# Kernel optimization log

Measured on AMD Instinct MI355X. Metric: run time of the kernel, lower is better.

The kernel has to match this reference:

```python
import jax, jax.numpy as jnp
from jax import lax
import numpy as np

B, N, C = 4, 2000, 80           # images, proposals/img, foreground classes
SCORE_THR = 0.05
IOU_THR = 0.5
MAX_PER_IMG = 100
K_PRE = 2000                     # pre-NMS top-k candidates per image
STDS = np.array([0.1, 0.1, 0.2, 0.2], dtype=np.float32)
MAX_RATIO = float(abs(np.log(16.0 / 1000.0)))  # wh_ratio_clip=16/1000


def setup_inputs() -> dict:
    key = jax.random.key(0)
    k1, k2, k3 = jax.random.split(key, 3)
    class_outs = jax.random.normal(k1, (B, N, C + 1), dtype=jnp.float32)
    regression_outs = jax.random.normal(k2, (B, N, C * 4), dtype=jnp.float32) * 0.5
    # random valid proposal boxes inside 800x1333 images (x1<x2, y1<y2)
    xy = jax.random.uniform(k3, (B, N, 2, 2), dtype=jnp.float32)
    xy = xy * jnp.array([1333.0, 800.0], dtype=jnp.float32)
    lo = jnp.min(xy, axis=2)
    hi = jnp.max(xy, axis=2) + 1.0
    boxes = jnp.concatenate([lo, hi], axis=-1)  # [B,N,4] x1,y1,x2,y2
    images_hw = jnp.tile(jnp.array([[800, 1333]], dtype=jnp.int32), (B, 1))
    return {"class_outs": class_outs, "regression_outs": regression_outs,
            "boxes": boxes, "images_hw": images_hw}


def _decode(props, deltas, h, w):
    # props [N,4], deltas [N,C,4] -> decoded boxes [N,C,4], clipped to image
    d = deltas * jnp.asarray(STDS)
    dx, dy, dw, dh = d[..., 0], d[..., 1], d[..., 2], d[..., 3]
    dw = jnp.clip(dw, -MAX_RATIO, MAX_RATIO)
    dh = jnp.clip(dh, -MAX_RATIO, MAX_RATIO)
    px = (props[:, None, 0] + props[:, None, 2]) * 0.5
    py = (props[:, None, 1] + props[:, None, 3]) * 0.5
    pw = props[:, None, 2] - props[:, None, 0]
    ph = props[:, None, 3] - props[:, None, 1]
    gx = px + pw * dx
    gy = py + ph * dy
    gw = pw * jnp.exp(dw)
    gh = ph * jnp.exp(dh)
    x1 = jnp.clip(gx - gw * 0.5, 0.0, w)
    y1 = jnp.clip(gy - gh * 0.5, 0.0, h)
    x2 = jnp.clip(gx + gw * 0.5, 0.0, w)
    y2 = jnp.clip(gy + gh * 0.5, 0.0, h)
    return jnp.stack([x1, y1, x2, y2], axis=-1)


def _pairwise_iou(b):
    # b [K,4] -> iou [K,K]
    area = (b[:, 2] - b[:, 0]) * (b[:, 3] - b[:, 1])
    lt = jnp.maximum(b[:, None, :2], b[None, :, :2])
    rb = jnp.minimum(b[:, None, 2:], b[None, :, 2:])
    wh = jnp.clip(rb - lt, 0.0)
    inter = wh[..., 0] * wh[..., 1]
    return inter / (area[:, None] + area[None, :] - inter + 1e-6)


def _process_image(cls_out, reg_out, props, hw):
    h = hw[0].astype(jnp.float32)
    w = hw[1].astype(jnp.float32)
    scores = jax.nn.softmax(cls_out, axis=-1)[:, :C]          # drop background col
    bboxes = _decode(props, reg_out.reshape(N, C, 4), h, w)   # [N,C,4]
    flat_scores = scores.reshape(-1)                          # [N*C]
    flat_boxes = bboxes.reshape(-1, 4)
    labels = jnp.tile(jnp.arange(C, dtype=jnp.int32), N)      # class fastest-varying
    cand = jnp.where(flat_scores > SCORE_THR, flat_scores, -1.0)
    top_scores, top_idx = lax.top_k(cand, K_PRE)
    top_boxes = flat_boxes[top_idx]
    top_labels = labels[top_idx]
    valid = top_scores > SCORE_THR
    # class-offset trick: boxes of distinct classes never overlap
    off = top_labels.astype(jnp.float32)[:, None] * (jnp.maximum(h, w) + 1.0)
    iou = _pairwise_iou(top_boxes + off)                      # [K_PRE,K_PRE]
    idxs = jnp.arange(K_PRE)

    def body(i, keep):
        sup = (idxs > i) & (iou[i] > IOU_THR) & keep[i]
        return keep & ~sup

    keep = lax.fori_loop(0, K_PRE, body, valid)
    kept_scores = jnp.where(keep, top_scores, -1.0)
    det_scores, det_i = lax.top_k(kept_scores, MAX_PER_IMG)
    det_valid = det_scores > SCORE_THR
    det_boxes = jnp.where(det_valid[:, None], top_boxes[det_i], 0.0)
    det_labels = jnp.where(det_valid, top_labels[det_i], -1)
    det_scores = jnp.where(det_valid, det_scores, 0.0)
    return det_boxes, det_scores, det_labels


def reference(class_outs, regression_outs, boxes, images_hw):
    det_boxes, det_scores, det_labels = jax.vmap(_process_image)(
        class_outs, regression_outs, boxes, images_hw)
    return det_boxes, det_scores, det_labels
```

## Files before the change

kernel.cpp:

```cpp
#include <hip/hip_runtime.h>


typedef unsigned long long u64;
typedef unsigned int u32;

#define B_ 4
#define N_ 2000
#define C_ 80
#define NCLS 81
#define KPRE 2000
#define MAXDET 100
#define TARGET 192
#define NB 2312
#define NBPAD 2368
#define NG 37
#define HBASE 0xF500
#define KSHIFT 46
#define CAPA 256
#define CAPB 2048
#define CAPBLK 128
#define BPI 125
#define SPW 9
#define BIGI 0x7fffffff

#define WS_GCNT  0
#define WS_GKEYS 2048
#define WS_GFLAG 514048
#define WS_GHIST 514064

__device__ __forceinline__ u64 pack_key(float score, unsigned fi) {
  return ((u64)__float_as_uint(score) << 32) | (u64)(0xFFFFFFFFu - fi);
}
__device__ __forceinline__ int bucket_of_bits(u32 sb) {
  return min(max((int)(sb >> 14) - HBASE, 0), NB - 1);
}

__device__ __forceinline__ float wred_max(float v) {
  int t;
#define STEPM(ctrl)                                                          \
  t = __builtin_amdgcn_update_dpp(__float_as_int(v), __float_as_int(v),      \
                                  (ctrl), 0xF, 0xF, false);                  \
  v = fmaxf(v, __int_as_float(t));
  STEPM(0x111) STEPM(0x112) STEPM(0x114) STEPM(0x118) STEPM(0x142) STEPM(0x143)
#undef STEPM
  return __int_as_float(__builtin_amdgcn_readlane(__float_as_int(v), 63));
}
__device__ __forceinline__ float wred_sum(float v) {
  int t;
#define STEPS(ctrl)                                                          \
  t = __builtin_amdgcn_update_dpp(0, __float_as_int(v), (ctrl), 0xF, 0xF,    \
                                  false);                                    \
  v = v + __int_as_float(t);
  STEPS(0x111) STEPS(0x112) STEPS(0x114) STEPS(0x118) STEPS(0x142) STEPS(0x143)
#undef STEPS
  return __int_as_float(__builtin_amdgcn_readlane(__float_as_int(v), 63));
}

__device__ __forceinline__ int dpp_min8(int v) {
  int t;
  t = __builtin_amdgcn_update_dpp(BIGI, v, 0x104, 0xF, 0xF, false);
  v = min(v, t);
  t = __builtin_amdgcn_update_dpp(BIGI, v, 0x102, 0xF, 0xF, false);
  v = min(v, t);
  t = __builtin_amdgcn_update_dpp(BIGI, v, 0x101, 0xF, 0xF, false);
  v = min(v, t);
  return v;
}

__device__ __forceinline__ float4 decode_one(
    u64 kk, const float* __restrict__ reg, const float* __restrict__ props,
    int b, float h, float w, float offscale) {
  const float MAXR = 4.135166556742356f;
  unsigned fi = 0xFFFFFFFFu - (u32)kk;
  int n = (int)(fi / (unsigned)C_);
  int c = (int)(fi - (unsigned)n * (unsigned)C_);
  float4 p = ((const float4*)props)[b * N_ + n];
  const float* dl = reg + ((size_t)(b * N_ + n)) * (C_ * 4) + c * 4;
  float dx = dl[0] * 0.1f;
  float dy = dl[1] * 0.1f;
  float dw = fminf(fmaxf(dl[2] * 0.2f, -MAXR), MAXR);
  float dh = fminf(fmaxf(dl[3] * 0.2f, -MAXR), MAXR);
  float px = (p.x + p.z) * 0.5f, py = (p.y + p.w) * 0.5f;
  float pw = p.z - p.x, ph = p.w - p.y;
  float gx = px + pw * dx, gy = py + ph * dy;
  float gw = pw * expf(dw), gh = ph * expf(dh);
  float off = (float)c * offscale;
  return make_float4(fminf(fmaxf(gx - gw * 0.5f, 0.0f), w) + off,
                     fminf(fmaxf(gy - gh * 0.5f, 0.0f), h) + off,
                     fminf(fmaxf(gx + gw * 0.5f, 0.0f), w) + off,
                     fminf(fmaxf(gy + gh * 0.5f, 0.0f), h) + off);
}

__global__ __launch_bounds__(1024) void cand_kernel(
    const float* __restrict__ cls, u64* __restrict__ gkeys,
    int* __restrict__ gcnt, u32* __restrict__ ghist) {
  __shared__ int s_wc[16], s_woff[16];
  const int tid = threadIdx.x;
  const int w = tid >> 6, lane = tid & 63;
  const int blk = blockIdx.x;
  const int b = blk / BPI;
  const int n = (blk % BPI) * 16 + w;
  const float* lg = cls + (size_t)(b * N_ + n) * NCLS;
  float x0 = lg[lane];
  float x1 = (lane < 17) ? lg[64 + lane] : -3.0e38f;
  float mx = wred_max(fmaxf(x0, x1));
  float e0 = expf(x0 - mx);
  float e1 = (lane < 17) ? expf(x1 - mx) : 0.0f;
  float sum = wred_sum(e0 + e1);
  float sc0 = e0 / sum, sc1 = e1 / sum;
  bool p0 = sc0 > 0.05f;
  bool p1 = (lane < 16) && (sc1 > 0.05f);
  u64 m0 = __ballot(p0), m1 = __ballot(p1);
  int c0 = __popcll(m0);
  if (lane == 0) s_wc[w] = c0 + __popcll(m1);
  __syncthreads();
  if (tid == 0) {
    int acc = 0;
#pragma unroll
    for (int i = 0; i < 16; ++i) { s_woff[i] = acc; acc += s_wc[i]; }
    gcnt[blk] = acc;
  }
  __syncthreads();
  const int base = s_woff[w];
  const u64 lt = (1ull << lane) - 1;
  u64* gk = gkeys + (size_t)blk * CAPBLK;
  u32* gh = ghist + (size_t)b * NBPAD;
  if (p0) {
    int slot = base + __popcll(m0 & lt);
    if (slot < CAPBLK) gk[slot] = pack_key(sc0, (unsigned)(n * C_ + lane));
    atomicAdd(&gh[bucket_of_bits(__float_as_uint(sc0))], 1u);
  }
  if (p1) {
    int slot = base + c0 + __popcll(m1 & lt);
    if (slot < CAPBLK) gk[slot] = pack_key(sc1, (unsigned)(n * C_ + 64 + lane));
    atomicAdd(&gh[bucket_of_bits(__float_as_uint(sc1))], 1u);
  }
}

__global__ __launch_bounds__(1024) void nmsA_kernel(
    const float* __restrict__ reg, const float* __restrict__ props,
    const int* __restrict__ hw, const u64* __restrict__ gkeys,
    const int* __restrict__ gcnt, const u32* __restrict__ ghist,
    int* __restrict__ gflag, float* __restrict__ out) {
  __shared__ u64 lds8[2156];
  char* bp = (char*)lds8;
  u64* SS = (u64*)bp;
  u64* U = (u64*)(bp + 2048);
  u64* rb = (u64*)(bp + 4128);
  float4* bxA = (float4*)(bp + 12320);
  int* outl = (int*)(bp + 16416);
  int* misc = (int*)(bp + 16928);
  int* s_coarse = (int*)(bp + 16992);

  const int b = blockIdx.x, tid = threadIdx.x;
  const int wv = tid >> 6, lane = tid & 63;

  float h = (float)hw[b * 2 + 0];
  float w = (float)hw[b * 2 + 1];
  float offscale = fmaxf(h, w) + 1.0f;

  if (tid < 16) misc[tid] = 0;
  if (tid >= NG && tid < 64) s_coarse[tid] = 0;

  int cnts[SPW];
  u64 ka[SPW], kb[SPW];
  if (wv < 14) {
#pragma unroll
    for (int k = 0; k < SPW; k++) {
      int p = wv * SPW + k;
      cnts[k] = (p < BPI) ? gcnt[b * BPI + p] : 0;
    }
#pragma unroll
    for (int k = 0; k < SPW; k++) {
      int p = wv * SPW + k;
      int cnt = min(cnts[k], CAPBLK);
      const u64* seg = gkeys + (size_t)(b * BPI + p) * CAPBLK;
      ka[k] = (lane < cnt) ? seg[lane] : 0ULL;
      kb[k] = (64 + lane < cnt) ? seg[64 + lane] : 0ULL;
    }
  } else {
    int g0 = (wv == 14) ? 0 : 19;
    int g1 = (wv == 14) ? 19 : NG;
    for (int g2 = g0; g2 < g1; g2++) {
      int v = (int)ghist[b * NBPAD + ((g2 << 6) | lane)];
#pragma unroll
      for (int o = 32; o; o >>= 1) v += __shfl_xor(v, o);
      if (lane == 0) s_coarse[g2] = v;
    }
  }
  __syncthreads();

  if (tid < 64) {
    int v = s_coarse[lane];
#pragma unroll
    for (int off = 1; off < 64; off <<= 1) {
      int src = lane + off;
      int o = __shfl(v, src < 64 ? src : 63);
      if (src < 64) v += o;
    }
    int Mtot = __shfl(v, 0);
    u64 pm = __ballot(v >= TARGET);
    int T_A = 0, S_A;
    if (pm) {
      int gs = 63 - __builtin_clzll(pm);
      int beyond = __shfl(v, gs + 1);
      int fv = (int)ghist[b * NBPAD + ((gs << 6) | lane)];
#pragma unroll
      for (int off = 1; off < 64; off <<= 1) {
        int src = lane + off;
        int o = __shfl(fv, src < 64 ? src : 63);
        if (src < 64) fv += o;
      }
      int cum = beyond + fv;
      u64 pm2 = __ballot(cum >= TARGET);
      int tr = 63 - __builtin_clzll(pm2);
      T_A = (gs << 6) + tr;
      S_A = __shfl(cum, tr);
    } else {
      S_A = Mtot;
    }
    if (lane == 0) { misc[0] = T_A; misc[2] = S_A; misc[3] = Mtot; }
  }
  __syncthreads();

  const int T_A = misc[0], S_A = misc[2], Mtot = misc[3];
  bool modeB = (S_A > CAPA);
  int K = 0, nkept = 0;

  if (!modeB) {
    if (wv < 14) {
      bool ovf = false;
      const u64 lt = (1ull << lane) - 1;
#pragma unroll
      for (int k = 0; k < SPW; k++) {
        int cnt = cnts[k];
        if (cnt > CAPBLK) { ovf = true; cnt = CAPBLK; }
        bool pr = (lane < cnt) &&
                  (bucket_of_bits((u32)(ka[k] >> 32)) >= T_A);
        u64 mk = __ballot(pr);
        if (mk) {
          int wbase = 0;
          if (lane == 0) wbase = atomicAdd(&misc[4], __popcll(mk));
          wbase = __shfl(wbase, 0);
          if (pr) {
            int pos = wbase + __popcll(mk & lt);
            if (pos < CAPA) U[pos] = ka[k];
          }
        }
        pr = (64 + lane < cnt) &&
             (bucket_of_bits((u32)(kb[k] >> 32)) >= T_A);
        mk = __ballot(pr);
        if (mk) {
          int wbase = 0;
          if (lane == 0) wbase = atomicAdd(&misc[4], __popcll(mk));
          wbase = __shfl(wbase, 0);
          if (pr) {
            int pos = wbase + __popcll(mk & lt);
            if (pos < CAPA) U[pos] = kb[k];
          }
        }
      }
      if (lane == 0 && ovf) misc[7] = 1;
    }
    __syncthreads();
    if (misc[7]) modeB = true;
    int S = misc[4];
    if (S > CAPA) S = CAPA;

    if (!modeB) {
      if (tid == 0 && (S & 1)) U[S] = 0ULL;
      __syncthreads();
      if (tid < S) {
        u64 k1 = U[tid];
        int r1 = 0;
        const ulonglong2* Uu2 = (const ulonglong2*)U;
        int half = (S + 1) >> 1;
        for (int k = 0; k < half; k++) {
          ulonglong2 kk = Uu2[k];
          r1 += (kk.x > k1) + (kk.y > k1);
        }
        SS[r1] = k1;
      }
      __syncthreads();
      K = S;
      for (int j = tid; j < K; j += 1024)
        bxA[j] = decode_one(SS[j], reg, props, b, h, w, offscale);
      __syncthreads();

      int nwords = (S + 63) >> 6;
      int ntiles = nwords * (nwords + 1) / 2;
      for (int t = wv; t < ntiles; t += 16) {
        int ti = 0, rem = t;
        while (rem >= nwords - ti) { rem -= nwords - ti; ti++; }
        int tj = ti + rem;
        int i = (ti << 6) + lane;
        float4 bi4 = bxA[i];
        float ai = (bi4.z - bi4.x) * (bi4.w - bi4.y);
        u64 bits = 0;
        int jbase = tj << 6;
        int jcount = min(64, S - jbase);
        for (int jj = 0; jj < jcount; jj++) {
          int j = jbase + jj;
          float4 bj = bxA[j];
          float aj = (bj.z - bj.x) * (bj.w - bj.y);
          float iw = fmaxf(fminf(bi4.z, bj.z) - fmaxf(bi4.x, bj.x), 0.0f);
          float ih = fmaxf(fminf(bi4.w, bj.w) - fmaxf(bi4.y, bj.y), 0.0f);
          float inter = iw * ih;
          float iou = inter / (ai + aj - inter + 1e-6f);
          if (j > i && iou > 0.5f) bits |= (1ull << jj);
        }
        if (i < S) rb[i * 4 + tj] = bits;
      }
      __syncthreads();

      if (tid < 64) {
        int nw7 = (S + 63) >> 6;
        u64 alive = 0;
        if (lane < nw7) {
          alive = ~0ull;
          int remb = S & 63;
          if (lane == nw7 - 1 && remb) alive = (1ull << remb) - 1;
        }
        int nk = 0;
        if (S > 0) {
          int i = 0;
          u64 row = (lane < nw7) ? rb[0 * 4 + lane] : 0ull;
          for (;;) {
            if (lane == 0) outl[nk] = i;
            nk++;
            if (nk >= MAXDET) break;
            if (lane == (i >> 6)) alive &= ~(1ull << (i & 63));
            u64 rowSpec = (i + 1 < S && lane < nw7) ? rb[(i + 1) * 4 + lane] : 0ull;
            u64 a2 = alive & ~row;
            alive = a2;
            int cnd = a2 ? ((lane << 6) + (int)__builtin_ctzll(a2)) : BIGI;
            int m8 = dpp_min8(cnd);
            int ni = __builtin_amdgcn_readfirstlane(m8);
            if (ni >= BIGI) break;
            row = (ni == i + 1) ? rowSpec
                                : ((lane < nw7) ? rb[ni * 4 + lane] : 0ull);
            i = ni;
          }
        }
        if (lane == 0) misc[6] = nk;
      }
      __syncthreads();
      nkept = misc[6];
      if (nkept < MAXDET && K < Mtot && K < KPRE) modeB = true;
    }
  }

  if (tid == 0) gflag[b] = modeB ? 1 : 0;
  if (modeB) return;

  float* oBox = out;
  float* oSc = out + B_ * MAXDET * 4;
  float* oLb = out + B_ * MAXDET * 5;
  for (int k2 = tid; k2 < MAXDET; k2 += 1024) {
    float4 bb = make_float4(0.0f, 0.0f, 0.0f, 0.0f);
    float sv = 0.0f, lv = -1.0f;
    if (k2 < nkept) {
      int idx = outl[k2];
      u64 kk = SS[idx];
      sv = __uint_as_float((u32)(kk >> 32));
      unsigned fi = 0xFFFFFFFFu - (u32)kk;
      int c = (int)(fi % (unsigned)C_);
      float off = (float)c * offscale;
      float4 ob = bxA[idx];
      bb = make_float4(ob.x - off, ob.y - off, ob.z - off, ob.w - off);
      lv = (float)c;
    }
    oBox[(b * MAXDET + k2) * 4 + 0] = bb.x;
    oBox[(b * MAXDET + k2) * 4 + 1] = bb.y;
    oBox[(b * MAXDET + k2) * 4 + 2] = bb.z;
    oBox[(b * MAXDET + k2) * 4 + 3] = bb.w;
    oSc[b * MAXDET + k2] = sv;
    oLb[b * MAXDET + k2] = lv;
  }
}

__global__ __launch_bounds__(1024) void nmsB_kernel(
    const float* __restrict__ reg, const float* __restrict__ props,
    const int* __restrict__ hw, const u64* __restrict__ gkeys,
    const int* __restrict__ gcnt, const int* __restrict__ gflag,
    float* __restrict__ out) {
  const int b = blockIdx.x, tid = threadIdx.x;
  if (gflag[b] == 0) return;

  __shared__ u64 lds8[7952];
  char* bp = (char*)lds8;
  u32* hist = (u32*)(bp + 0);
  u64* U2 = (u64*)(bp + 9472);
  u64* SSB = (u64*)(bp + 25856);
  int* outl = (int*)(bp + 42240);
  int* misc = (int*)(bp + 42752);
  const int wv = tid >> 6, lane = tid & 63;

  float h = (float)hw[b * 2 + 0];
  float w = (float)hw[b * 2 + 1];
  float offscale = fmaxf(h, w) + 1.0f;

  for (int i = tid; i < NBPAD; i += 1024) hist[i] = 0;
  if (tid < 16) misc[tid] = 0;
  __syncthreads();

  for (int k = 0; k < 8; k++) {
    int p = wv + 16 * k;
    if (p >= BPI) break;
    int cnt = min(gcnt[b * BPI + p], CAPBLK);
    const u64* seg = gkeys + (size_t)(b * BPI + p) * CAPBLK;
#pragma unroll
    for (int r = 0; r < 2; r++) {
      int idx = lane + 64 * r;
      if (idx < cnt) {
        u64 key = seg[idx];
        int bi = min(max((int)(key >> KSHIFT) - HBASE, 0), NB - 1);
        atomicAdd(&hist[bi], 1u);
      }
    }
  }
  __syncthreads();

  if (tid == 0) {
    int acc = 0, tb = 0;
    for (int bi = NB - 1; bi >= 0; bi--) {
      acc += (int)hist[bi];
      if (acc >= KPRE) { tb = bi; break; }
    }
    if (acc > CAPB) tb = min(tb + 1, NB - 1);
    misc[1] = tb;
    misc[4] = 0;
  }
  __syncthreads();
  int T_B = misc[1];

  for (int k = 0; k < 8; k++) {
    int p = wv + 16 * k;
    if (p >= BPI) break;
    int cnt = min(gcnt[b * BPI + p], CAPBLK);
    const u64* seg = gkeys + (size_t)(b * BPI + p) * CAPBLK;
#pragma unroll
    for (int r = 0; r < 2; r++) {
      int idx = lane + 64 * r;
      bool pred = false;
      u64 key = 0;
      if (idx < cnt) {
        key = seg[idx];
        int bi = min(max((int)(key >> KSHIFT) - HBASE, 0), NB - 1);
        pred = (bi >= T_B);
      }
      u64 mk = __ballot(pred);
      if (mk) {
        int wbase = 0;
        if (lane == 0) wbase = atomicAdd(&misc[4], __popcll(mk));
        wbase = __shfl(wbase, 0);
        if (pred) {
          int pos = wbase + __popcll(mk & ((1ull << lane) - 1));
          if (pos < CAPB) U2[pos] = key;
        }
      }
    }
  }
  __syncthreads();
  int S = misc[4];
  if (S > CAPB) S = CAPB;
  {
    int j1 = tid, j2 = tid + 1024;
    u64 k1 = (j1 < S) ? U2[j1] : 0ULL;
    u64 k2 = (j2 < S) ? U2[j2] : 0ULL;
    int r1 = 0, r2 = 0;
    for (int k = 0; k < S; k++) {
      u64 kk = U2[k];
      r1 += (kk > k1);
      r2 += (kk > k2);
    }
    __syncthreads();
    if (j1 < S) SSB[r1] = k1;
    if (j2 < S) SSB[r2] = k2;
  }
  __syncthreads();
  int K = (S < KPRE) ? S : KPRE;
  int j1 = tid, j2 = tid + 1024;
  bool kp1 = (j1 < K), kp2 = (j2 < K);
  float4 bb1 = kp1 ? decode_one(SSB[j1], reg, props, b, h, w, offscale)
                   : make_float4(0, 0, 0, 0);
  float4 bb2 = kp2 ? decode_one(SSB[j2], reg, props, b, h, w, offscale)
                   : make_float4(0, 0, 0, 0);
  int nk = 0;
  if (K > 0) {
    int i = 0;
    for (;;) {
      if (tid == 0) { outl[nk] = i; misc[5] = K; }
      nk++;
      if (nk >= MAXDET) break;
      __syncthreads();
      float4 tb = decode_one(SSB[i], reg, props, b, h, w, offscale);
      float ai = (tb.z - tb.x) * (tb.w - tb.y);
      int ln = K;
      if (kp1 && j1 > i) {
        float aj = (bb1.z - bb1.x) * (bb1.w - bb1.y);
        float iw = fmaxf(fminf(tb.z, bb1.z) - fmaxf(tb.x, bb1.x), 0.0f);
        float ih = fmaxf(fminf(tb.w, bb1.w) - fmaxf(tb.y, bb1.y), 0.0f);
        float inter = iw * ih;
        float iou = inter / (ai + aj - inter + 1e-6f);
        if (iou > 0.5f) kp1 = false;
        else ln = min(ln, j1);
      }
      if (kp2 && j2 > i) {
        float aj = (bb2.z - bb2.x) * (bb2.w - bb2.y);
        float iw = fmaxf(fminf(tb.z, bb2.z) - fmaxf(tb.x, bb2.x), 0.0f);
        float ih = fmaxf(fminf(tb.w, bb2.w) - fmaxf(tb.y, bb2.y), 0.0f);
        float inter = iw * ih;
        float iou = inter / (ai + aj - inter + 1e-6f);
        if (iou > 0.5f) kp2 = false;
        else ln = min(ln, j2);
      }
#pragma unroll
      for (int off = 32; off; off >>= 1) ln = min(ln, __shfl_xor(ln, off));
      if ((tid & 63) == 0 && ln < K) atomicMin(&misc[5], ln);
      __syncthreads();
      int ni = misc[5];
      __syncthreads();
      if (ni >= K) break;
      i = ni;
    }
  }
  if (tid == 0) misc[6] = nk;
  __syncthreads();
  int nkept = misc[6];

  float* oBox = out;
  float* oSc = out + B_ * MAXDET * 4;
  float* oLb = out + B_ * MAXDET * 5;
  for (int k2 = tid; k2 < MAXDET; k2 += 1024) {
    float4 bb = make_float4(0.0f, 0.0f, 0.0f, 0.0f);
    float sv = 0.0f, lv = -1.0f;
    if (k2 < nkept) {
      int idx = outl[k2];
      u64 kk = SSB[idx];
      sv = __uint_as_float((u32)(kk >> 32));
      unsigned fi = 0xFFFFFFFFu - (u32)kk;
      int c = (int)(fi % (unsigned)C_);
      float off = (float)c * offscale;
      float4 ob = decode_one(kk, reg, props, b, h, w, offscale);
      bb = make_float4(ob.x - off, ob.y - off, ob.z - off, ob.w - off);
      lv = (float)c;
    }
    oBox[(b * MAXDET + k2) * 4 + 0] = bb.x;
    oBox[(b * MAXDET + k2) * 4 + 1] = bb.y;
    oBox[(b * MAXDET + k2) * 4 + 2] = bb.z;
    oBox[(b * MAXDET + k2) * 4 + 3] = bb.w;
    oSc[b * MAXDET + k2] = sv;
    oLb[b * MAXDET + k2] = lv;
  }
}

extern "C" void kernel_launch(void* const* d_in, const int* in_sizes, int n_in,
                              void* d_out, int out_size, void* d_ws, size_t ws_size,
                              hipStream_t stream) {
  const float* cls = (const float*)d_in[0];
  const float* reg = (const float*)d_in[1];
  const float* props = (const float*)d_in[2];
  const int* hw = (const int*)d_in[3];
  float* out = (float*)d_out;

  int* gcnt = (int*)((char*)d_ws + WS_GCNT);
  u64* gkeys = (u64*)((char*)d_ws + WS_GKEYS);
  int* gflag = (int*)((char*)d_ws + WS_GFLAG);
  u32* ghist = (u32*)((char*)d_ws + WS_GHIST);

  hipMemsetAsync(ghist, 0, (size_t)B_ * NBPAD * 4, stream);
  cand_kernel<<<B_ * BPI, 1024, 0, stream>>>(cls, gkeys, gcnt, ghist);
  nmsA_kernel<<<B_, 1024, 0, stream>>>(reg, props, hw, gkeys, gcnt, ghist,
                                       gflag, out);
  nmsB_kernel<<<B_, 1024, 0, stream>>>(reg, props, hw, gkeys, gcnt, gflag, out);
}
```

Before: 112.4 us.

## Compact candidate keys per image via global atomic cursor instead of per-block segments

```diff
diff --git a/kernel.cpp b/kernel.cpp
--- a/kernel.cpp
+++ b/kernel.cpp
@@ -18,15 +18,16 @@
 #define KSHIFT 46
 #define CAPA 256
 #define CAPB 2048
-#define CAPBLK 128
+#define CAPIMG 8192
+#define KPT 8
 #define BPI 125
-#define SPW 9
 #define BIGI 0x7fffffff
 
-#define WS_GCNT  0
-#define WS_GKEYS 2048
-#define WS_GFLAG 514048
-#define WS_GHIST 514064
+#define WS_GCUR  0
+#define WS_GHIST 64
+#define WS_GFLAG 37952
+#define WS_GKEYS 38016
+#define WS_ZEND  37952
 
 __device__ __forceinline__ u64 pack_key(float score, unsigned fi) {
   return ((u64)__float_as_uint(score) << 32) | (u64)(0xFFFFFFFFu - fi);
@@ -93,8 +94,9 @@
 
 __global__ __launch_bounds__(1024) void cand_kernel(
     const float* __restrict__ cls, u64* __restrict__ gkeys,
-    int* __restrict__ gcnt, u32* __restrict__ ghist) {
+    u32* __restrict__ gcur, u32* __restrict__ ghist) {
   __shared__ int s_wc[16], s_woff[16];
+  __shared__ int s_base;
   const int tid = threadIdx.x;
   const int w = tid >> 6, lane = tid & 63;
   const int blk = blockIdx.x;
@@ -118,21 +120,21 @@
     int acc = 0;
 #pragma unroll
     for (int i = 0; i < 16; ++i) { s_woff[i] = acc; acc += s_wc[i]; }
-    gcnt[blk] = acc;
-  }
-  __syncthreads();
-  const int base = s_woff[w];
+    s_base = (acc > 0) ? (int)atomicAdd(&gcur[b], (u32)acc) : 0;
+  }
+  __syncthreads();
+  const int base = s_base + s_woff[w];
   const u64 lt = (1ull << lane) - 1;
-  u64* gk = gkeys + (size_t)blk * CAPBLK;
+  u64* gk = gkeys + (size_t)b * CAPIMG;
   u32* gh = ghist + (size_t)b * NBPAD;
   if (p0) {
     int slot = base + __popcll(m0 & lt);
-    if (slot < CAPBLK) gk[slot] = pack_key(sc0, (unsigned)(n * C_ + lane));
+    if (slot < CAPIMG) gk[slot] = pack_key(sc0, (unsigned)(n * C_ + lane));
     atomicAdd(&gh[bucket_of_bits(__float_as_uint(sc0))], 1u);
   }
   if (p1) {
     int slot = base + c0 + __popcll(m1 & lt);
-    if (slot < CAPBLK) gk[slot] = pack_key(sc1, (unsigned)(n * C_ + 64 + lane));
+    if (slot < CAPIMG) gk[slot] = pack_key(sc1, (unsigned)(n * C_ + 64 + lane));
     atomicAdd(&gh[bucket_of_bits(__float_as_uint(sc1))], 1u);
   }
 }
@@ -140,7 +142,7 @@
 __global__ __launch_bounds__(1024) void nmsA_kernel(
     const float* __restrict__ reg, const float* __restrict__ props,
     const int* __restrict__ hw, const u64* __restrict__ gkeys,
-    const int* __restrict__ gcnt, const u32* __restrict__ ghist,
+    const u32* __restrict__ gcur, const u32* __restrict__ ghist,
     int* __restrict__ gflag, float* __restrict__ out) {
   __shared__ u64 lds8[2156];
   char* bp = (char*)lds8;
@@ -162,25 +164,19 @@
   if (tid < 16) misc[tid] = 0;
   if (tid >= NG && tid < 64) s_coarse[tid] = 0;
 
-  int cnts[SPW];
-  u64 ka[SPW], kb[SPW];
-  if (wv < 14) {
-#pragma unroll
-    for (int k = 0; k < SPW; k++) {
-      int p = wv * SPW + k;
-      cnts[k] = (p < BPI) ? gcnt[b * BPI + p] : 0;
-    }
-#pragma unroll
-    for (int k = 0; k < SPW; k++) {
-      int p = wv * SPW + k;
-      int cnt = min(cnts[k], CAPBLK);
-      const u64* seg = gkeys + (size_t)(b * BPI + p) * CAPBLK;
-      ka[k] = (lane < cnt) ? seg[lane] : 0ULL;
-      kb[k] = (64 + lane < cnt) ? seg[64 + lane] : 0ULL;
-    }
-  } else {
-    int g0 = (wv == 14) ? 0 : 19;
-    int g1 = (wv == 14) ? 19 : NG;
+  const u64* keys = gkeys + (size_t)b * CAPIMG;
+  const u32 Mraw = gcur[b];
+  const int M = min((int)Mraw, CAPIMG);
+  if (tid == 0 && Mraw > (u32)CAPIMG) misc[7] = 1;
+  u64 kreg[KPT];
+#pragma unroll
+  for (int r = 0; r < KPT; r++) {
+    int idx = tid + (r << 10);
+    kreg[r] = (idx < M) ? keys[idx] : 0ULL;
+  }
+  if (wv >= 12) {
+    int g0 = (wv == 12) ? 0 : 10 + (wv - 13) * 9;
+    int g1 = (wv == 12) ? 10 : g0 + 9;
     for (int g2 = g0; g2 < g1; g2++) {
       int v = (int)ghist[b * NBPAD + ((g2 << 6) | lane)];
 #pragma unroll
@@ -224,19 +220,17 @@
   __syncthreads();
 
   const int T_A = misc[0], S_A = misc[2], Mtot = misc[3];
-  bool modeB = (S_A > CAPA);
+  bool modeB = (S_A > CAPA) || (misc[7] != 0);
   int K = 0, nkept = 0;
 
   if (!modeB) {
-    if (wv < 14) {
-      bool ovf = false;
+    {
       const u64 lt = (1ull << lane) - 1;
 #pragma unroll
-      for (int k = 0; k < SPW; k++) {
-        int cnt = cnts[k];
-        if (cnt > CAPBLK) { ovf = true; cnt = CAPBLK; }
-        bool pr = (lane < cnt) &&
-                  (bucket_of_bits((u32)(ka[k] >> 32)) >= T_A);
+      for (int r = 0; r < KPT; r++) {
+        int idx = tid + (r << 10);
+        bool pr = (idx < M) &&
+                  (bucket_of_bits((u32)(kreg[r] >> 32)) >= T_A);
         u64 mk = __ballot(pr);
         if (mk) {
           int wbase = 0;
@@ -244,110 +238,94 @@
           wbase = __shfl(wbase, 0);
           if (pr) {
             int pos = wbase + __popcll(mk & lt);
-            if (pos < CAPA) U[pos] = ka[k];
+            if (pos < CAPA) U[pos] = kreg[r];
           }
         }
-        pr = (64 + lane < cnt) &&
-             (bucket_of_bits((u32)(kb[k] >> 32)) >= T_A);
-        mk = __ballot(pr);
-        if (mk) {
-          int wbase = 0;
-          if (lane == 0) wbase = atomicAdd(&misc[4], __popcll(mk));
-          wbase = __shfl(wbase, 0);
-          if (pr) {
-            int pos = wbase + __popcll(mk & lt);
-            if (pos < CAPA) U[pos] = kb[k];
-          }
-        }
-      }
-      if (lane == 0 && ovf) misc[7] = 1;
-    }
-    __syncthreads();
-    if (misc[7]) modeB = true;
+      }
+    }
+    __syncthreads();
     int S = misc[4];
     if (S > CAPA) S = CAPA;
 
-    if (!modeB) {
-      if (tid == 0 && (S & 1)) U[S] = 0ULL;
-      __syncthreads();
-      if (tid < S) {
-        u64 k1 = U[tid];
-        int r1 = 0;
-        const ulonglong2* Uu2 = (const ulonglong2*)U;
-        int half = (S + 1) >> 1;
-        for (int k = 0; k < half; k++) {
-          ulonglong2 kk = Uu2[k];
-          r1 += (kk.x > k1) + (kk.y > k1);
+    if (tid == 0 && (S & 1)) U[S] = 0ULL;
+    __syncthreads();
+    if (tid < S) {
+      u64 k1 = U[tid];
+      int r1 = 0;
+      const ulonglong2* Uu2 = (const ulonglong2*)U;
+      int half = (S + 1) >> 1;
+      for (int k = 0; k < half; k++) {
+        ulonglong2 kk = Uu2[k];
+        r1 += (kk.x > k1) + (kk.y > k1);
+      }
+      SS[r1] = k1;
+    }
+    __syncthreads();
+    K = S;
+    for (int j = tid; j < K; j += 1024)
+      bxA[j] = decode_one(SS[j], reg, props, b, h, w, offscale);
+    __syncthreads();
+
+    int nwords = (S + 63) >> 6;
+    int ntiles = nwords * (nwords + 1) / 2;
+    for (int t = wv; t < ntiles; t += 16) {
+      int ti = 0, rem = t;
+      while (rem >= nwords - ti) { rem -= nwords - ti; ti++; }
+      int tj = ti + rem;
+      int i = (ti << 6) + lane;
+      float4 bi4 = bxA[i];
+      float ai = (bi4.z - bi4.x) * (bi4.w - bi4.y);
+      u64 bits = 0;
+      int jbase = tj << 6;
+      int jcount = min(64, S - jbase);
+      for (int jj = 0; jj < jcount; jj++) {
+        int j = jbase + jj;
+        float4 bj = bxA[j];
+        float aj = (bj.z - bj.x) * (bj.w - bj.y);
+        float iw = fmaxf(fminf(bi4.z, bj.z) - fmaxf(bi4.x, bj.x), 0.0f);
+        float ih = fmaxf(fminf(bi4.w, bj.w) - fmaxf(bi4.y, bj.y), 0.0f);
+        float inter = iw * ih;
+        float iou = inter / (ai + aj - inter + 1e-6f);
+        if (j > i && iou > 0.5f) bits |= (1ull << jj);
+      }
+      if (i < S) rb[i * 4 + tj] = bits;
+    }
+    __syncthreads();
+
+    if (tid < 64) {
+      int nw7 = (S + 63) >> 6;
+      u64 alive = 0;
+      if (lane < nw7) {
+        alive = ~0ull;
+        int remb = S & 63;
+        if (lane == nw7 - 1 && remb) alive = (1ull << remb) - 1;
+      }
+      int nk = 0;
+      if (S > 0) {
+        int i = 0;
+        u64 row = (lane < nw7) ? rb[0 * 4 + lane] : 0ull;
+        for (;;) {
+          if (lane == 0) outl[nk] = i;
+          nk++;
+          if (nk >= MAXDET) break;
+          if (lane == (i >> 6)) alive &= ~(1ull << (i & 63));
+          u64 rowSpec = (i + 1 < S && lane < nw7) ? rb[(i + 1) * 4 + lane] : 0ull;
+          u64 a2 = alive & ~row;
+          alive = a2;
+          int cnd = a2 ? ((lane << 6) + (int)__builtin_ctzll(a2)) : BIGI;
+          int m8 = dpp_min8(cnd);
+          int ni = __builtin_amdgcn_readfirstlane(m8);
+          if (ni >= BIGI) break;
+          row = (ni == i + 1) ? rowSpec
+                              : ((lane < nw7) ? rb[ni * 4 + lane] : 0ull);
+          i = ni;
         }
-        SS[r1] = k1;
-      }
-      __syncthreads();
-      K = S;
-      for (int j = tid; j < K; j += 1024)
-        bxA[j] = decode_one(SS[j], reg, props, b, h, w, offscale);
-      __syncthreads();
-
-      int nwords = (S + 63) >> 6;
-      int ntiles = nwords * (nwords + 1) / 2;
-      for (int t = wv; t < ntiles; t += 16) {
-        int ti = 0, rem = t;
-        while (rem >= nwords - ti) { rem -= nwords - ti; ti++; }
-        int tj = ti + rem;
-        int i = (ti << 6) + lane;
-        float4 bi4 = bxA[i];
-        float ai = (bi4.z - bi4.x) * (bi4.w - bi4.y);
-        u64 bits = 0;
-        int jbase = tj << 6;
-        int jcount = min(64, S - jbase);
-        for (int jj = 0; jj < jcount; jj++) {
-          int j = jbase + jj;
-          float4 bj = bxA[j];
-          float aj = (bj.z - bj.x) * (bj.w - bj.y);
-          float iw = fmaxf(fminf(bi4.z, bj.z) - fmaxf(bi4.x, bj.x), 0.0f);
-          float ih = fmaxf(fminf(bi4.w, bj.w) - fmaxf(bi4.y, bj.y), 0.0f);
-          float inter = iw * ih;
-          float iou = inter / (ai + aj - inter + 1e-6f);
-          if (j > i && iou > 0.5f) bits |= (1ull << jj);
-        }
-        if (i < S) rb[i * 4 + tj] = bits;
-      }
-      __syncthreads();
-
-      if (tid < 64) {
-        int nw7 = (S + 63) >> 6;
-        u64 alive = 0;
-        if (lane < nw7) {
-          alive = ~0ull;
-          int remb = S & 63;
-          if (lane == nw7 - 1 && remb) alive = (1ull << remb) - 1;
-        }
-        int nk = 0;
-        if (S > 0) {
-          int i = 0;
-          u64 row = (lane < nw7) ? rb[0 * 4 + lane] : 0ull;
-          for (;;) {
-            if (lane == 0) outl[nk] = i;
-            nk++;
-            if (nk >= MAXDET) break;
-            if (lane == (i >> 6)) alive &= ~(1ull << (i & 63));
-            u64 rowSpec = (i + 1 < S && lane < nw7) ? rb[(i + 1) * 4 + lane] : 0ull;
-            u64 a2 = alive & ~row;
-            alive = a2;
-            int cnd = a2 ? ((lane << 6) + (int)__builtin_ctzll(a2)) : BIGI;
-            int m8 = dpp_min8(cnd);
-            int ni = __builtin_amdgcn_readfirstlane(m8);
-            if (ni >= BIGI) break;
-            row = (ni == i + 1) ? rowSpec
-                                : ((lane < nw7) ? rb[ni * 4 + lane] : 0ull);
-            i = ni;
-          }
-        }
-        if (lane == 0) misc[6] = nk;
-      }
-      __syncthreads();
-      nkept = misc[6];
-      if (nkept < MAXDET && K < Mtot && K < KPRE) modeB = true;
-    }
+      }
+      if (lane == 0) misc[6] = nk;
+    }
+    __syncthreads();
+    nkept = misc[6];
+    if (nkept < MAXDET && K < Mtot && K < KPRE) modeB = true;
   }
 
   if (tid == 0) gflag[b] = modeB ? 1 : 0;
@@ -382,7 +360,7 @@
 __global__ __launch_bounds__(1024) void nmsB_kernel(
     const float* __restrict__ reg, const float* __restrict__ props,
     const int* __restrict__ hw, const u64* __restrict__ gkeys,
-    const int* __restrict__ gcnt, const int* __restrict__ gflag,
+    const u32* __restrict__ gcur, const int* __restrict__ gflag,
     float* __restrict__ out) {
   const int b = blockIdx.x, tid = threadIdx.x;
   if (gflag[b] == 0) return;
@@ -394,30 +372,23 @@
   u64* SSB = (u64*)(bp + 25856);
   int* outl = (int*)(bp + 42240);
   int* misc = (int*)(bp + 42752);
-  const int wv = tid >> 6, lane = tid & 63;
+  const int lane = tid & 63;
 
   float h = (float)hw[b * 2 + 0];
   float w = (float)hw[b * 2 + 1];
   float offscale = fmaxf(h, w) + 1.0f;
 
+  const u64* keys = gkeys + (size_t)b * CAPIMG;
+  const int M = min((int)gcur[b], CAPIMG);
+
   for (int i = tid; i < NBPAD; i += 1024) hist[i] = 0;
   if (tid < 16) misc[tid] = 0;
   __syncthreads();
 
-  for (int k = 0; k < 8; k++) {
-    int p = wv + 16 * k;
-    if (p >= BPI) break;
-    int cnt = min(gcnt[b * BPI + p], CAPBLK);
-    const u64* seg = gkeys + (size_t)(b * BPI + p) * CAPBLK;
-#pragma unroll
-    for (int r = 0; r < 2; r++) {
-      int idx = lane + 64 * r;
-      if (idx < cnt) {
-        u64 key = seg[idx];
-        int bi = min(max((int)(key >> KSHIFT) - HBASE, 0), NB - 1);
-        atomicAdd(&hist[bi], 1u);
-      }
-    }
+  for (int idx = tid; idx < M; idx += 1024) {
+    u64 key = keys[idx];
+    int bi = min(max((int)(key >> KSHIFT) - HBASE, 0), NB - 1);
+    atomicAdd(&hist[bi], 1u);
   }
   __syncthreads();
 
@@ -434,30 +405,23 @@
   __syncthreads();
   int T_B = misc[1];
 
-  for (int k = 0; k < 8; k++) {
-    int p = wv + 16 * k;
-    if (p >= BPI) break;
-    int cnt = min(gcnt[b * BPI + p], CAPBLK);
-    const u64* seg = gkeys + (size_t)(b * BPI + p) * CAPBLK;
-#pragma unroll
-    for (int r = 0; r < 2; r++) {
-      int idx = lane + 64 * r;
-      bool pred = false;
-      u64 key = 0;
-      if (idx < cnt) {
-        key = seg[idx];
-        int bi = min(max((int)(key >> KSHIFT) - HBASE, 0), NB - 1);
-        pred = (bi >= T_B);
-      }
-      u64 mk = __ballot(pred);
-      if (mk) {
-        int wbase = 0;
-        if (lane == 0) wbase = atomicAdd(&misc[4], __popcll(mk));
-        wbase = __shfl(wbase, 0);
-        if (pred) {
-          int pos = wbase + __popcll(mk & ((1ull << lane) - 1));
-          if (pos < CAPB) U2[pos] = key;
-        }
+  for (int idx0 = 0; idx0 < M; idx0 += 1024) {
+    int idx = idx0 + tid;
+    bool pred = false;
+    u64 key = 0;
+    if (idx < M) {
+      key = keys[idx];
+      int bi = min(max((int)(key >> KSHIFT) - HBASE, 0), NB - 1);
+      pred = (bi >= T_B);
+    }
+    u64 mk = __ballot(pred);
+    if (mk) {
+      int wbase = 0;
+      if (lane == 0) wbase = atomicAdd(&misc[4], __popcll(mk));
+      wbase = __shfl(wbase, 0);
+      if (pred) {
+        int pos = wbase + __popcll(mk & ((1ull << lane) - 1));
+        if (pos < CAPB) U2[pos] = key;
       }
     }
   }
@@ -564,14 +528,14 @@
   const int* hw = (const int*)d_in[3];
   float* out = (float*)d_out;
 
-  int* gcnt = (int*)((char*)d_ws + WS_GCNT);
+  u32* gcur = (u32*)((char*)d_ws + WS_GCUR);
+  u32* ghist = (u32*)((char*)d_ws + WS_GHIST);
+  int* gflag = (int*)((char*)d_ws + WS_GFLAG);
   u64* gkeys = (u64*)((char*)d_ws + WS_GKEYS);
-  int* gflag = (int*)((char*)d_ws + WS_GFLAG);
-  u32* ghist = (u32*)((char*)d_ws + WS_GHIST);
-
-  hipMemsetAsync(ghist, 0, (size_t)B_ * NBPAD * 4, stream);
-  cand_kernel<<<B_ * BPI, 1024, 0, stream>>>(cls, gkeys, gcnt, ghist);
-  nmsA_kernel<<<B_, 1024, 0, stream>>>(reg, props, hw, gkeys, gcnt, ghist,
+
+  hipMemsetAsync(d_ws, 0, WS_ZEND, stream);
+  cand_kernel<<<B_ * BPI, 1024, 0, stream>>>(cls, gkeys, gcur, ghist);
+  nmsA_kernel<<<B_, 1024, 0, stream>>>(reg, props, hw, gkeys, gcur, ghist,
                                        gflag, out);
-  nmsB_kernel<<<B_, 1024, 0, stream>>>(reg, props, hw, gkeys, gcnt, gflag, out);
-}
+  nmsB_kernel<<<B_, 1024, 0, stream>>>(reg, props, hw, gkeys, gcur, gflag, out);
+}
```

Measured after the change: 109.5 us. -2.6%, faster.
